# Kernel optimization log

Hardware: AMD Instinct MI355X
Metric: run time of the kernel (lower is better)

The kernel has to match this reference:

```python
import jax, jax.numpy as jnp
import numpy as np

B, IN, H, N, W, K = 32, 256, 512, 32768, 64, 8
EPS = 1e-12  # torch F.normalize eps


def setup_inputs() -> dict:
    key = jax.random.key(0)
    ks = jax.random.split(key, 16)
    inp = {
        "x": jax.random.normal(ks[0], (B, IN), jnp.float32),
        "h_prev": jax.random.normal(ks[1], (B, H), jnp.float32),
        "c_prev": jax.random.normal(ks[2], (B, H), jnp.float32),
        "M_prev": jax.random.normal(ks[3], (B, N, W), jnp.float32),
        "wr_prev": jax.random.uniform(ks[4], (B, N), jnp.float32),
        "usage_prev": jax.random.uniform(ks[5], (B, N), jnp.float32),
        "r_prev": jax.random.normal(ks[6], (B, W), jnp.float32),
        # LSTMCell params (torch layout: [4H, in] / [4H, H], gate order i,f,g,o)
        "W_ih": jax.random.normal(ks[7], (4 * H, IN + W), jnp.float32) * 0.02,
        "W_hh": jax.random.normal(ks[8], (4 * H, H), jnp.float32) * 0.02,
        "b_ih": jax.random.normal(ks[9], (4 * H,), jnp.float32) * 0.02,
        "b_hh": jax.random.normal(ks[10], (4 * H,), jnp.float32) * 0.02,
        # output_projector: hidden -> 3W + 2
        "W_proj": jax.random.normal(ks[11], (3 * W + 2, H), jnp.float32) * 0.02,
        "b_proj": jax.random.normal(ks[12], (3 * W + 2,), jnp.float32) * 0.02,
        # final_projector: hidden + W -> hidden
        "W_final": jax.random.normal(ks[13], (H, H + W), jnp.float32) * 0.02,
        "b_final": jax.random.normal(ks[14], (H,), jnp.float32) * 0.02,
    }
    return inp


def _l2norm(v, axis):
    n = jnp.sqrt(jnp.sum(v * v, axis=axis, keepdims=True))
    return v / jnp.maximum(n, EPS)


def reference(x, h_prev, c_prev, M_prev, wr_prev, usage_prev, r_prev,
              W_ih, W_hh, b_ih, b_hh, W_proj, b_proj, W_final, b_final):
    # ---- LSTM controller step ----
    lstm_in = jnp.concatenate([x, r_prev], axis=1)            # [B, IN+W]
    gates = lstm_in @ W_ih.T + b_ih + h_prev @ W_hh.T + b_hh  # [B, 4H]
    gi, gf, gg, go = jnp.split(gates, 4, axis=1)
    i = jax.nn.sigmoid(gi)
    f = jax.nn.sigmoid(gf)
    g = jnp.tanh(gg)
    o = jax.nn.sigmoid(go)
    c_curr = f * c_prev + i * g
    h_curr = o * jnp.tanh(c_curr)

    # ---- interface params ----
    params = h_curr @ W_proj.T + b_proj                       # [B, 3W+2]
    q = params[:, :W]
    a = params[:, W:2 * W]
    e = jax.nn.sigmoid(params[:, 2 * W:3 * W])
    alpha = jax.nn.sigmoid(params[:, -2:-1])                  # [B,1]
    gamma = jax.nn.sigmoid(params[:, -1:])                    # [B,1]

    # ---- sparse read: cosine sim -> topK -> scattered softmax ----
    q_n = _l2norm(q, axis=1)                                  # [B, W]
    m_n = _l2norm(M_prev, axis=2)                             # [B, N, W]
    sim = jnp.einsum('bw,bnw->bn', q_n, m_n)                  # [B, N]
    top_vals, top_idx = jax.lax.top_k(sim, K)                 # [B, K]
    sm = jax.nn.softmax(top_vals, axis=1)                     # softmax(-inf elsewhere) == 0
    b_idx = jnp.arange(sim.shape[0])[:, None]
    w_r = jnp.zeros_like(sim).at[b_idx, top_idx].set(sm)      # [B, N]
    r_curr = jnp.einsum('bn,bnw->bw', w_r, M_prev)            # [B, W]

    # ---- usage / LRU write weights ----
    usage_curr = usage_prev + 1.0
    access_mask = jnp.zeros_like(usage_curr).at[b_idx, top_idx].set(1.0)
    usage_curr = usage_curr * (1.0 - access_mask)
    lru = jnp.argmax(usage_curr, axis=1)                      # [B]
    I_U = jax.nn.one_hot(lru, usage_curr.shape[1], dtype=usage_curr.dtype)
    w_w = alpha * (gamma * wr_prev + (1.0 - gamma) * I_U)     # [B, N]

    # ---- rank-1 erase / add memory update ----
    w_w_exp = w_w[:, :, None]                                 # [B, N, 1]
    M_curr = M_prev * (1.0 - w_w_exp * e[:, None, :]) + w_w_exp * a[:, None, :]

    # ---- output ----
    y_out = jnp.concatenate([h_curr, r_curr], axis=1) @ W_final.T + b_final
    return (y_out, h_curr, c_curr, M_curr, w_r, usage_curr, r_curr)
```

## Files before the change

### kernel.cpp

```cpp
#include <hip/hip_runtime.h>
#include <math.h>

#define B_ 32
#define IN_ 256
#define H_ 512
#define N_ 32768
#define W_ 64
#define K_ 8
#define PROJ_ 194
#define NCHUNK 128

typedef float f32x4 __attribute__((ext_vector_type(4)));

#define OUT_Y  0
#define OUT_H  16384
#define OUT_C  32768
#define OUT_M  49152
#define OUT_WR 67158016
#define OUT_US 68206592
#define OUT_R  69255168

#define WS_QN    0
#define WS_AA    2048
#define WS_EE    4096
#define WS_ALPHA 6144
#define WS_GAMMA 6176
#define WS_LRU   6208
#define WS_CVAL  8192
#define WS_CIDX  40960

__device__ __forceinline__ float sigmoidf_(float v) { return 1.f / (1.f + expf(-v)); }

__global__ __launch_bounds__(256) void k_lstm(
    const float* __restrict__ x, const float* __restrict__ r_prev,
    const float* __restrict__ h_prev, const float* __restrict__ c_prev,
    const float* __restrict__ W_ih, const float* __restrict__ W_hh,
    const float* __restrict__ b_ih, const float* __restrict__ b_hh,
    float* __restrict__ h_out, float* __restrict__ c_out) {
  int wid = (blockIdx.x * blockDim.x + threadIdx.x) >> 6;
  int lane = threadIdx.x & 63;
  if (wid >= B_ * H_) return;
  int b = wid >> 9;
  int h = wid & (H_ - 1);
  float a0 = 0.f, a1 = 0.f, a2 = 0.f, a3 = 0.f;
  const float4* x4 = (const float4*)(x + b * IN_);
  const float4* r4 = (const float4*)(r_prev + b * W_);
  for (int c = lane; c < 80; c += 64) {
    float4 in4 = (c < 64) ? x4[c] : r4[c - 64];
    #pragma unroll
    for (int g = 0; g < 4; ++g) {
      float4 w4 = ((const float4*)(W_ih + (size_t)(g * H_ + h) * 320))[c];
      float d = fmaf(w4.x, in4.x, fmaf(w4.y, in4.y, fmaf(w4.z, in4.z, w4.w * in4.w)));
      if (g == 0) a0 += d; else if (g == 1) a1 += d; else if (g == 2) a2 += d; else a3 += d;
    }
  }
  const float4* h4 = (const float4*)(h_prev + b * H_);
  for (int c = lane; c < 128; c += 64) {
    float4 in4 = h4[c];
    #pragma unroll
    for (int g = 0; g < 4; ++g) {
      float4 w4 = ((const float4*)(W_hh + (size_t)(g * H_ + h) * 512))[c];
      float d = fmaf(w4.x, in4.x, fmaf(w4.y, in4.y, fmaf(w4.z, in4.z, w4.w * in4.w)));
      if (g == 0) a0 += d; else if (g == 1) a1 += d; else if (g == 2) a2 += d; else a3 += d;
    }
  }
  #pragma unroll
  for (int m = 1; m < 64; m <<= 1) {
    a0 += __shfl_xor(a0, m); a1 += __shfl_xor(a1, m);
    a2 += __shfl_xor(a2, m); a3 += __shfl_xor(a3, m);
  }
  if (lane == 0) {
    float gi = a0 + b_ih[h] + b_hh[h];
    float gf = a1 + b_ih[H_ + h] + b_hh[H_ + h];
    float gg = a2 + b_ih[2 * H_ + h] + b_hh[2 * H_ + h];
    float go = a3 + b_ih[3 * H_ + h] + b_hh[3 * H_ + h];
    float i_ = sigmoidf_(gi), f_ = sigmoidf_(gf), g_ = tanhf(gg), o_ = sigmoidf_(go);
    float cc = f_ * c_prev[b * H_ + h] + i_ * g_;
    c_out[b * H_ + h] = cc;
    h_out[b * H_ + h] = o_ * tanhf(cc);
  }
}

__global__ __launch_bounds__(256) void k_projpost(
    const float* __restrict__ h_curr, const float* __restrict__ W_proj,
    const float* __restrict__ b_proj, float* __restrict__ qn,
    float* __restrict__ aa, float* __restrict__ ee,
    float* __restrict__ alpha, float* __restrict__ gamma) {
  int b = blockIdx.x, tid = threadIdx.x;
  int wave = tid >> 6, lane = tid & 63;
  __shared__ float params[PROJ_];
  const float4* h4 = (const float4*)(h_curr + b * H_);
  float4 ha = h4[lane], hb = h4[lane + 64];
  for (int p = wave; p < PROJ_; p += 4) {
    const float4* w4p = (const float4*)(W_proj + (size_t)p * H_);
    float4 wa = w4p[lane], wb = w4p[lane + 64];
    float acc = fmaf(wa.x, ha.x, fmaf(wa.y, ha.y, fmaf(wa.z, ha.z, wa.w * ha.w)))
              + fmaf(wb.x, hb.x, fmaf(wb.y, hb.y, fmaf(wb.z, hb.z, wb.w * hb.w)));
    #pragma unroll
    for (int m = 1; m < 64; m <<= 1) acc += __shfl_xor(acc, m);
    if (lane == 0) params[p] = acc + b_proj[p];
  }
  __syncthreads();
  if (tid < W_) {
    float q = params[tid];
    float s = q * q;
    #pragma unroll
    for (int m = 1; m < 64; m <<= 1) s += __shfl_xor(s, m);
    float nrm = fmaxf(sqrtf(s), 1e-12f);
    qn[b * W_ + tid] = q / nrm;
    aa[b * W_ + tid] = params[W_ + tid];
    ee[b * W_ + tid] = sigmoidf_(params[2 * W_ + tid]);
    if (tid == 0) alpha[b] = sigmoidf_(params[192]);
    if (tid == 1) gamma[b] = sigmoidf_(params[193]);
  }
}

__global__ __launch_bounds__(256) void k_simupd(
    const float* __restrict__ M, const float* __restrict__ qn,
    const float* __restrict__ wr_prev, const float* __restrict__ aa,
    const float* __restrict__ ee, const float* __restrict__ alpha,
    const float* __restrict__ gamma, float* __restrict__ M_out,
    float* __restrict__ cval, int* __restrict__ cidx, float* __restrict__ w_r) {
  int b = blockIdx.y, chunk = blockIdx.x, tid = threadIdx.x;
  int j = tid & 15;
  __builtin_nontemporal_store(0.f, &w_r[(size_t)b * N_ + chunk * 256 + tid]);
  __shared__ float simv[256];
  __shared__ float wv[4]; __shared__ int wi[4];
  const float* Mb = M + ((size_t)b * N_ + (size_t)chunk * 256) * W_;
  float* Ob = M_out + ((size_t)b * N_ + (size_t)chunk * 256) * W_;
  const float* wrb = wr_prev + (size_t)b * N_ + chunk * 256;
  float4 q4 = ((const float4*)(qn + b * W_))[j];
  float4 e4 = ((const float4*)(ee + b * W_))[j];
  float4 a4 = ((const float4*)(aa + b * W_))[j];
  float c0 = alpha[b] * gamma[b];
  #pragma unroll 4
  for (int it = 0; it < 16; ++it) {
    float4 m4 = *(const float4*)(Mb + (size_t)it * 1024 + tid * 4);
    int r = it * 16 + (tid >> 4);
    float ww = c0 * wrb[r];
    f32x4 o;
    o.x = fmaf(m4.x, 1.f - ww * e4.x, ww * a4.x);
    o.y = fmaf(m4.y, 1.f - ww * e4.y, ww * a4.y);
    o.z = fmaf(m4.z, 1.f - ww * e4.z, ww * a4.z);
    o.w = fmaf(m4.w, 1.f - ww * e4.w, ww * a4.w);
    __builtin_nontemporal_store(o, (f32x4*)(Ob + (size_t)it * 1024 + tid * 4));
    float dot = fmaf(m4.x, q4.x, fmaf(m4.y, q4.y, fmaf(m4.z, q4.z, m4.w * q4.w)));
    float sq  = fmaf(m4.x, m4.x, fmaf(m4.y, m4.y, fmaf(m4.z, m4.z, m4.w * m4.w)));
    #pragma unroll
    for (int m = 1; m < 16; m <<= 1) { dot += __shfl_xor(dot, m); sq += __shfl_xor(sq, m); }
    if (j == 0) simv[r] = dot / fmaxf(sqrtf(sq), 1e-12f);
  }
  __syncthreads();
  float v = simv[tid];
  int idx = chunk * 256 + tid;
  float myv = 0.f; int myi = 0;
  for (int sel = 0; sel < K_; ++sel) {
    float bv = v; int bi = idx;
    #pragma unroll
    for (int m = 1; m < 64; m <<= 1) {
      float ov = __shfl_xor(bv, m); int oi = __shfl_xor(bi, m);
      if (ov > bv || (ov == bv && oi < bi)) { bv = ov; bi = oi; }
    }
    if ((tid & 63) == 0) { wv[tid >> 6] = bv; wi[tid >> 6] = bi; }
    __syncthreads();
    float gv = wv[0]; int gi = wi[0];
    #pragma unroll
    for (int w = 1; w < 4; ++w) {
      float ov = wv[w]; int oi = wi[w];
      if (ov > gv || (ov == gv && oi < gi)) { gv = ov; gi = oi; }
    }
    if (idx == gi) v = -INFINITY;
    if (tid == sel) { myv = gv; myi = gi; }
    __syncthreads();
  }
  if (tid < K_) {
    cval[((size_t)b * NCHUNK + chunk) * K_ + tid] = myv;
    cidx[((size_t)b * NCHUNK + chunk) * K_ + tid] = myi;
  }
}

__global__ __launch_bounds__(1024) void k_muse(
    const float* __restrict__ cval, const int* __restrict__ cidx,
    const float* __restrict__ M, const float* __restrict__ usage_prev,
    float* __restrict__ usage_out, float* __restrict__ r_out,
    float* __restrict__ w_r, int* __restrict__ lru) {
  int b = blockIdx.x, tid = threadIdx.x;
  __shared__ float wv[16]; __shared__ int wi[16];
  float v = cval[(size_t)b * NCHUNK * K_ + tid];
  int idx = cidx[(size_t)b * NCHUNK * K_ + tid];
  float topv[K_]; int topi[K_];
  #pragma unroll
  for (int sel = 0; sel < K_; ++sel) {
    float bv = v; int bi = idx;
    #pragma unroll
    for (int m = 1; m < 64; m <<= 1) {
      float ov = __shfl_xor(bv, m); int oi = __shfl_xor(bi, m);
      if (ov > bv || (ov == bv && oi < bi)) { bv = ov; bi = oi; }
    }
    if ((tid & 63) == 0) { wv[tid >> 6] = bv; wi[tid >> 6] = bi; }
    __syncthreads();
    float gv = wv[0]; int gi = wi[0];
    #pragma unroll
    for (int w = 1; w < 16; ++w) {
      float ov = wv[w]; int oi = wi[w];
      if (ov > gv || (ov == gv && oi < gi)) { gv = ov; gi = oi; }
    }
    if (idx == gi) v = -INFINITY;
    topv[sel] = gv; topi[sel] = gi;
    __syncthreads();
  }
  float mx = topv[0], ssum = 0.f, e[K_];
  #pragma unroll
  for (int k = 0; k < K_; ++k) { e[k] = expf(topv[k] - mx); ssum += e[k]; }
  #pragma unroll
  for (int k = 0; k < K_; ++k) e[k] /= ssum;
  if (tid < K_) w_r[(size_t)b * N_ + topi[tid]] = e[tid];
  if (tid < W_) {
    float acc = 0.f;
    #pragma unroll
    for (int k = 0; k < K_; ++k)
      acc += e[k] * M[((size_t)b * N_ + (size_t)topi[k]) * W_ + tid];
    r_out[b * W_ + tid] = acc;
  }
  const f32x4* up = (const f32x4*)(usage_prev + (size_t)b * N_);
  f32x4* uo = (f32x4*)(usage_out + (size_t)b * N_);
  float bu = -1.f; int bn = 0x7fffffff;
  for (int i = tid; i < N_ / 4; i += 1024) {
    f32x4 u = up[i];
    int n0 = i * 4;
    float uu[4] = {u.x + 1.f, u.y + 1.f, u.z + 1.f, u.w + 1.f};
    #pragma unroll
    for (int c = 0; c < 4; ++c) {
      int n = n0 + c;
      bool acc = false;
      #pragma unroll
      for (int k = 0; k < K_; ++k) acc |= (n == topi[k]);
      if (acc) uu[c] = 0.f;
      if (uu[c] > bu || (uu[c] == bu && n < bn)) { bu = uu[c]; bn = n; }
    }
    f32x4 w = {uu[0], uu[1], uu[2], uu[3]};
    __builtin_nontemporal_store(w, &uo[i]);
  }
  #pragma unroll
  for (int m = 1; m < 64; m <<= 1) {
    float ov = __shfl_xor(bu, m); int oi = __shfl_xor(bn, m);
    if (ov > bu || (ov == bu && oi < bn)) { bu = ov; bn = oi; }
  }
  if ((tid & 63) == 0) { wv[tid >> 6] = bu; wi[tid >> 6] = bn; }
  __syncthreads();
  if (tid == 0) {
    float gv = wv[0]; int gi = wi[0];
    #pragma unroll
    for (int w = 1; w < 16; ++w) {
      float ov = wv[w]; int oi = wi[w];
      if (ov > gv || (ov == gv && oi < gi)) { gv = ov; gi = oi; }
    }
    lru[b] = gi;
  }
}

__global__ void k_fix(
    const float* __restrict__ M, const float* __restrict__ wr_prev,
    const float* __restrict__ aa, const float* __restrict__ ee,
    const float* __restrict__ alpha, const float* __restrict__ gamma,
    const int* __restrict__ lru, float* __restrict__ M_out) {
  int b = blockIdx.x, t = threadIdx.x;
  int n = lru[b];
  float al = alpha[b], ga = gamma[b];
  float ww = al * (ga * wr_prev[(size_t)b * N_ + n] + (1.f - ga));
  float e = ee[b * W_ + t], a = aa[b * W_ + t];
  float m = M[((size_t)b * N_ + n) * W_ + t];
  M_out[((size_t)b * N_ + n) * W_ + t] = fmaf(m, 1.f - ww * e, ww * a);
}

__global__ __launch_bounds__(256) void k_yout(
    const float* __restrict__ h_curr, const float* __restrict__ r_curr,
    const float* __restrict__ W_final, const float* __restrict__ b_final,
    float* __restrict__ y) {
  int wid = (blockIdx.x * blockDim.x + threadIdx.x) >> 6;
  int lane = threadIdx.x & 63;
  if (wid >= B_ * H_) return;
  int b = wid >> 9;
  int o = wid & (H_ - 1);
  float acc = 0.f;
  const float4* h4 = (const float4*)(h_curr + b * H_);
  const float4* r4 = (const float4*)(r_curr + b * W_);
  const float4* w4p = (const float4*)(W_final + (size_t)o * 576);
  for (int c = lane; c < 144; c += 64) {
    float4 in4 = (c < 128) ? h4[c] : r4[c - 128];
    float4 w4 = w4p[c];
    acc += fmaf(w4.x, in4.x, fmaf(w4.y, in4.y, fmaf(w4.z, in4.z, w4.w * in4.w)));
  }
  #pragma unroll
  for (int m = 1; m < 64; m <<= 1) acc += __shfl_xor(acc, m);
  if (lane == 0) y[b * H_ + o] = acc + b_final[o];
}

extern "C" void kernel_launch(void* const* d_in, const int* in_sizes, int n_in,
                              void* d_out, int out_size, void* d_ws, size_t ws_size,
                              hipStream_t stream) {
  const float* x          = (const float*)d_in[0];
  const float* h_prev     = (const float*)d_in[1];
  const float* c_prev     = (const float*)d_in[2];
  const float* M_prev     = (const float*)d_in[3];
  const float* wr_prev    = (const float*)d_in[4];
  const float* usage_prev = (const float*)d_in[5];
  const float* r_prev     = (const float*)d_in[6];
  const float* W_ih       = (const float*)d_in[7];
  const float* W_hh       = (const float*)d_in[8];
  const float* b_ih       = (const float*)d_in[9];
  const float* b_hh       = (const float*)d_in[10];
  const float* W_proj     = (const float*)d_in[11];
  const float* b_proj     = (const float*)d_in[12];
  const float* W_final    = (const float*)d_in[13];
  const float* b_final    = (const float*)d_in[14];

  float* out   = (float*)d_out;
  float* y_out = out + OUT_Y;
  float* h_out = out + OUT_H;
  float* c_out = out + OUT_C;
  float* M_out = out + OUT_M;
  float* wr_out = out + OUT_WR;
  float* us_out = out + OUT_US;
  float* r_out  = out + OUT_R;

  float* ws    = (float*)d_ws;
  float* qn    = ws + WS_QN;
  float* aa    = ws + WS_AA;
  float* ee    = ws + WS_EE;
  float* alpha = ws + WS_ALPHA;
  float* gamma = ws + WS_GAMMA;
  int*   lru   = (int*)(ws + WS_LRU);
  float* cval  = ws + WS_CVAL;
  int*   cidx  = (int*)(ws + WS_CIDX);

  k_lstm<<<4096, 256, 0, stream>>>(x, r_prev, h_prev, c_prev, W_ih, W_hh, b_ih, b_hh,
                                   h_out, c_out);
  k_projpost<<<32, 256, 0, stream>>>(h_out, W_proj, b_proj, qn, aa, ee, alpha, gamma);
  dim3 sg(NCHUNK, B_);
  k_simupd<<<sg, 256, 0, stream>>>(M_prev, qn, wr_prev, aa, ee, alpha, gamma,
                                   M_out, cval, cidx, wr_out);
  k_muse<<<32, 1024, 0, stream>>>(cval, cidx, M_prev, usage_prev, us_out, r_out,
                                  wr_out, lru);
  k_fix<<<32, 64, 0, stream>>>(M_prev, wr_prev, aa, ee, alpha, gamma, lru, M_out);
  k_yout<<<4096, 256, 0, stream>>>(h_out, r_out, W_final, b_final, y_out);
}
```

Measured before the change: 183.6 us.

## Enlarge sim chunks to 1024 rows with per-wave top-k and no block syncs

Each block now handles 1024 memory rows instead of 256, cutting the grid from 128 to 32 chunks per batch. Top-k inside a block is done per wave over 256 rows, each lane holding 4 values in registers, so the block-wide shared-memory reductions and barriers are gone. Each wave writes 8 candidates, which still gives 1024 candidates per batch for the merge kernel. The cost is fewer blocks (1024 in total) and longer per-block loops, which may hurt latency hiding on a bandwidth-bound streaming kernel.

New measurement: 189.8 us. 1.03x slower.

```diff
diff --git a/kernel.cpp b/kernel.cpp
--- a/kernel.cpp
+++ b/kernel.cpp
@@ -8,7 +8,9 @@
 #define W_ 64
 #define K_ 8
 #define PROJ_ 194
-#define NCHUNK 128
+#define NCHUNK 32
+#define CROWS 1024
+#define NCAND 1024
 
 typedef float f32x4 __attribute__((ext_vector_type(4)));
 
@@ -123,18 +125,18 @@
     float* __restrict__ cval, int* __restrict__ cidx, float* __restrict__ w_r) {
   int b = blockIdx.y, chunk = blockIdx.x, tid = threadIdx.x;
   int j = tid & 15;
-  __builtin_nontemporal_store(0.f, &w_r[(size_t)b * N_ + chunk * 256 + tid]);
-  __shared__ float simv[256];
-  __shared__ float wv[4]; __shared__ int wi[4];
-  const float* Mb = M + ((size_t)b * N_ + (size_t)chunk * 256) * W_;
-  float* Ob = M_out + ((size_t)b * N_ + (size_t)chunk * 256) * W_;
-  const float* wrb = wr_prev + (size_t)b * N_ + chunk * 256;
+  __shared__ float simv[CROWS];
+  f32x4 z = {0.f, 0.f, 0.f, 0.f};
+  __builtin_nontemporal_store(z, (f32x4*)(w_r + (size_t)b * N_ + chunk * CROWS + tid * 4));
+  const float* Mb = M + ((size_t)b * N_ + (size_t)chunk * CROWS) * W_;
+  float* Ob = M_out + ((size_t)b * N_ + (size_t)chunk * CROWS) * W_;
+  const float* wrb = wr_prev + (size_t)b * N_ + chunk * CROWS;
   float4 q4 = ((const float4*)(qn + b * W_))[j];
   float4 e4 = ((const float4*)(ee + b * W_))[j];
   float4 a4 = ((const float4*)(aa + b * W_))[j];
   float c0 = alpha[b] * gamma[b];
-  #pragma unroll 4
-  for (int it = 0; it < 16; ++it) {
+  #pragma unroll 8
+  for (int it = 0; it < 64; ++it) {
     float4 m4 = *(const float4*)(Mb + (size_t)it * 1024 + tid * 4);
     int r = it * 16 + (tid >> 4);
     float ww = c0 * wrb[r];
@@ -151,31 +153,36 @@
     if (j == 0) simv[r] = dot / fmaxf(sqrtf(sq), 1e-12f);
   }
   __syncthreads();
-  float v = simv[tid];
-  int idx = chunk * 256 + tid;
+  int wave = tid >> 6, lane = tid & 63;
+  int rbase = wave * 256 + lane;
+  float v0 = simv[rbase];
+  float v1 = simv[rbase + 64];
+  float v2 = simv[rbase + 128];
+  float v3 = simv[rbase + 192];
+  int base = chunk * CROWS + rbase;
   float myv = 0.f; int myi = 0;
+  #pragma unroll
   for (int sel = 0; sel < K_; ++sel) {
-    float bv = v; int bi = idx;
+    float bv = v0; int bk = 0;
+    if (v1 > bv) { bv = v1; bk = 1; }
+    if (v2 > bv) { bv = v2; bk = 2; }
+    if (v3 > bv) { bv = v3; bk = 3; }
+    int bi = base + (bk << 6);
     #pragma unroll
     for (int m = 1; m < 64; m <<= 1) {
       float ov = __shfl_xor(bv, m); int oi = __shfl_xor(bi, m);
       if (ov > bv || (ov == bv && oi < bi)) { bv = ov; bi = oi; }
     }
-    if ((tid & 63) == 0) { wv[tid >> 6] = bv; wi[tid >> 6] = bi; }
-    __syncthreads();
-    float gv = wv[0]; int gi = wi[0];
-    #pragma unroll
-    for (int w = 1; w < 4; ++w) {
-      float ov = wv[w]; int oi = wi[w];
-      if (ov > gv || (ov == gv && oi < gi)) { gv = ov; gi = oi; }
-    }
-    if (idx == gi) v = -INFINITY;
-    if (tid == sel) { myv = gv; myi = gi; }
-    __syncthreads();
-  }
-  if (tid < K_) {
-    cval[((size_t)b * NCHUNK + chunk) * K_ + tid] = myv;
-    cidx[((size_t)b * NCHUNK + chunk) * K_ + tid] = myi;
+    if (bi == base)            v0 = -INFINITY;
+    else if (bi == base + 64)  v1 = -INFINITY;
+    else if (bi == base + 128) v2 = -INFINITY;
+    else if (bi == base + 192) v3 = -INFINITY;
+    if (lane == sel) { myv = bv; myi = bi; }
+  }
+  if (lane < K_) {
+    size_t co = ((size_t)(b * NCHUNK + chunk) * 4 + wave) * K_ + lane;
+    cval[co] = myv;
+    cidx[co] = myi;
   }
 }
 
@@ -186,8 +193,8 @@
     float* __restrict__ w_r, int* __restrict__ lru) {
   int b = blockIdx.x, tid = threadIdx.x;
   __shared__ float wv[16]; __shared__ int wi[16];
-  float v = cval[(size_t)b * NCHUNK * K_ + tid];
-  int idx = cidx[(size_t)b * NCHUNK * K_ + tid];
+  float v = cval[(size_t)b * NCAND + tid];
+  int idx = cidx[(size_t)b * NCAND + tid];
   float topv[K_]; int topi[K_];
   #pragma unroll
   for (int sel = 0; sel < K_; ++sel) {
```
